# Performance work log

Hardware: AMD Instinct MI355X
Metric: run time of the kernel (lower is better)

Reference implementation:

```python
import jax, jax.numpy as jnp
import numpy as np

B = 65536
X_DIM = 362
A = 3  # action_space / number of expert dynamics MLPs


def setup_inputs() -> dict:
    key = jax.random.key(0)
    ks = jax.random.split(key, 12)
    batch_x = jax.random.normal(ks[0], (B, X_DIM), dtype=jnp.float32)
    batch_next = jax.random.normal(ks[1], (B, X_DIM), dtype=jnp.float32)
    # Plant the pointer sentinel (value 10.0) at a random in-bounds grid cell per row,
    # so that ptr-19 >= 0 and ptr+19 < X_DIM (grid width is 19).
    ptr_pos = jax.random.randint(ks[2], (B,), 20, 343)
    batch_x = batch_x.at[jnp.arange(B), ptr_pos].set(10.0)
    batch_a = jax.random.randint(ks[3], (B,), 0, A, dtype=jnp.int32)

    def lin(k, fan_in, shape):
        return (jax.random.normal(k, shape, dtype=jnp.float32) / np.sqrt(fan_in)).astype(jnp.float32)

    W1 = lin(ks[4], 6, (A, 6, 100));   b1 = jnp.zeros((A, 100), jnp.float32)
    W2 = lin(ks[5], 100, (A, 100, 400)); b2 = jnp.zeros((A, 400), jnp.float32)
    W3 = lin(ks[6], 400, (A, 400, 100)); b3 = jnp.zeros((A, 100), jnp.float32)
    W4 = lin(ks[7], 100, (A, 100, 6));  b4 = jnp.zeros((A, 6), jnp.float32)
    return {"batch_x": batch_x, "batch_next": batch_next, "batch_a": batch_a,
            "W1": W1, "b1": b1, "W2": W2, "b2": b2, "W3": W3, "b3": b3, "W4": W4, "b4": b4}


def _attend(data, ptr):
    # cell_list = [0, p, p-19 (left), p+19 (right), p-1 (above), p+1 (below)]
    zeros = jnp.zeros_like(ptr)
    idx = jnp.stack([zeros, ptr, ptr - 19, ptr + 19, ptr - 1, ptr + 1], axis=1)  # [B, 6]
    return jnp.take_along_axis(data, idx, axis=1)  # [B, 6]


def _expert(x, a, W1, b1, W2, b2, W3, b3, W4, b4):
    h = jax.nn.relu(x @ W1[a] + b1[a])
    h = jax.nn.relu(h @ W2[a] + b2[a])
    h = jax.nn.relu(h @ W3[a] + b3[a])
    return h @ W4[a] + b4[a]


def reference(batch_x, batch_next, batch_a, W1, b1, W2, b2, W3, b3, W4, b4):
    # Pointer index = first occurrence of sentinel value 10.0 per row.
    ptr = jnp.argmax(batch_x == 10.0, axis=1)  # [B]
    att = _attend(batch_x, ptr)        # [B, 6]
    att_next = _attend(batch_next, ptr)  # [B, 6]
    # Per-action routed expert MLPs (A is small and fixed): compute each expert
    # over the batch and select per-sample by action id.
    preds = jnp.zeros_like(att)
    for a in range(A):
        out_a = _expert(att, a, W1, b1, W2, b2, W3, b3, W4, b4)
        preds = jnp.where((batch_a == a)[:, None], out_a, preds)
    actual_deltas = att_next - att
    return jnp.mean((preds - actual_deltas) ** 2)
```

## Files before the change

kernel.cpp:

```cpp
#include <hip/hip_runtime.h>
#include <hip/hip_bf16.h>

#define B_ROWS 65536
#define XD 362

typedef __bf16 bf16;
typedef __attribute__((ext_vector_type(8))) __bf16 bf16x8;
typedef __attribute__((ext_vector_type(4))) float f32x4;
typedef __attribute__((ext_vector_type(2))) float f32x2;

#define MFMA16(A, Bf, C) __builtin_amdgcn_mfma_f32_16x16x32_bf16(A, Bf, C, 0, 0, 0)
#define ORDER() __builtin_amdgcn_sched_barrier(0x7F)

#define OFF_W1T   0u
#define OFF_W2T   21504u
#define OFF_W3T   340992u
#define OFF_W4T   620544u
#define OFF_CNT   632832u
#define OFF_PTR   633088u
#define OFF_ATTC  895232u
#define OFF_DELTA 4040960u
#define OFF_PART  8759552u

#define MLP_GRID 520
#define WPREP_BLOCKS 624
#define SCAN_BLOCKS 2896

__global__ __launch_bounds__(256) void k_prep(
    const float* __restrict__ W1, const float* __restrict__ b1,
    const float* __restrict__ W2, const float* __restrict__ b2,
    const float* __restrict__ W3, const float* __restrict__ b3,
    const float* __restrict__ W4, const float* __restrict__ b4,
    const float* __restrict__ x,
    bf16* __restrict__ W1t, bf16* __restrict__ W2t,
    bf16* __restrict__ W3t, bf16* __restrict__ W4t,
    int* __restrict__ cnt, int* __restrict__ ptrArr)
{
  int bx = blockIdx.x;
  if (bx >= WPREP_BLOCKS) {
    int gid = (bx - WPREP_BLOCKS) * 256 + threadIdx.x;
    const float4* x4 = (const float4*)x;
#pragma unroll
    for (int u = 0; u < 8; ++u) {
      int i = gid + u * (SCAN_BLOCKS * 256);
      float4 v = x4[i];
      if (v.x == 10.0f || v.y == 10.0f || v.z == 10.0f || v.w == 10.0f) {
        int flat = i * 4;
        if (v.x == 10.0f) ptrArr[(flat    ) / XD] = (flat    ) % XD;
        if (v.y == 10.0f) ptrArr[(flat + 1) / XD] = (flat + 1) % XD;
        if (v.z == 10.0f) ptrArr[(flat + 2) / XD] = (flat + 2) % XD;
        if (v.w == 10.0f) ptrArr[(flat + 3) / XD] = (flat + 3) % XD;
      }
    }
    return;
  }
  int i = bx * 256 + threadIdx.x;
  if (i == 0) { cnt[0] = 0; cnt[1] = 0; cnt[2] = 0; }
  if (i < 3*416*128) {
    int k = i & 127; int rn = i >> 7; int n = rn % 416; int a = rn / 416;
    float v = 0.f;
    if (n < 400) {
      if (k < 100) v = W2[(a*100 + k)*400 + n];
      else if (k == 100) v = b2[a*400 + n];
    } else if (n == 400) {
      v = (k == 100) ? 1.0f : 0.0f;
    }
    W2t[i] = (bf16)v;
  }
  if (i < 3*112*416) {
    int k = i % 416; int rn = i / 416; int n = rn % 112; int a = rn / 112;
    float v = 0.f;
    if (n < 100) {
      if (k < 400) v = W3[(a*400 + k)*100 + n];
      else if (k == 400) v = b3[a*100 + n];
    }
    W3t[i] = (bf16)v;
  }
  if (i < 3*112*32) {
    int k = i & 31; int rn = i >> 5; int n = rn % 112; int a = rn / 112;
    float v = 0.f;
    if (n < 100) {
      if (k < 6) v = W1[(a*6 + k)*100 + n];
      else if (k == 6) v = b1[a*100 + n];
    }
    W1t[i] = (bf16)v;
  }
  if (i < 3*16*128) {
    int k = i & 127; int rn = i >> 7; int n = rn & 15; int a = rn >> 4;
    float v = 0.f;
    if (n < 6) {
      if (k < 100) v = W4[(a*100 + k)*6 + n];
      else if (k == 100) v = b4[a*6 + n];
    }
    W4t[i] = (bf16)v;
  }
}

__global__ __launch_bounds__(256) void k_gather2(
    const float* __restrict__ x, const float* __restrict__ xn,
    const int* __restrict__ act, const int* __restrict__ ptrArr,
    bf16* __restrict__ attC, float* __restrict__ deltaC, int* __restrict__ cnt)
{
  int row = blockIdx.x * 256 + threadIdx.x;
  int lane = threadIdx.x & 63;
  int p = ptrArr[row];
  if (p < 20 || p > 342) p = 20;
  const float* xr = x  + (size_t)row * XD;
  const float* nr = xn + (size_t)row * XD;
  int cells[6] = {0, p, p - 19, p + 19, p - 1, p + 1};
  float av[6], dv[6];
#pragma unroll
  for (int i = 0; i < 6; ++i) {
    av[i] = xr[cells[i]];
    dv[i] = nr[cells[i]] - av[i];
  }
  int a = act[row];
  unsigned long long m0 = __ballot(a == 0);
  unsigned long long m1 = __ballot(a == 1);
  unsigned long long m2 = __ballot(a == 2);
  int b0 = 0, b1 = 0, b2 = 0;
  if (lane == 0) {
    b0 = atomicAdd(&cnt[0], (int)__popcll(m0));
    b1 = atomicAdd(&cnt[1], (int)__popcll(m1));
    b2 = atomicAdd(&cnt[2], (int)__popcll(m2));
  }
  b0 = __shfl(b0, 0); b1 = __shfl(b1, 0); b2 = __shfl(b2, 0);
  unsigned long long lt = (1ull << lane) - 1ull;
  unsigned long long ma = (a == 0) ? m0 : (a == 1) ? m1 : m2;
  int base            = (a == 0) ? b0 : (a == 1) ? b1 : b2;
  int slot = base + (int)__popcll(ma & lt);
  size_t rb = (size_t)a * B_ROWS + slot;
  bf16x8 av8;
#pragma unroll
  for (int i = 0; i < 6; ++i) av8[i] = (bf16)av[i];
  av8[6] = (bf16)1.0f;
  av8[7] = (bf16)0.0f;
  *(bf16x8*)(attC + rb * 8) = av8;
  f32x2 d01 = {dv[0], dv[1]}, d23 = {dv[2], dv[3]}, d45 = {dv[4], dv[5]};
  *(f32x2*)(deltaC + rb * 6)     = d01;
  *(f32x2*)(deltaC + rb * 6 + 2) = d23;
  *(f32x2*)(deltaC + rb * 6 + 4) = d45;
}

__global__ __launch_bounds__(256, 2) void k_mlp(
    const bf16* __restrict__ W1t, const bf16* __restrict__ W2t,
    const bf16* __restrict__ W3t, const bf16* __restrict__ W4t,
    const bf16* __restrict__ attC, const float* __restrict__ deltaC,
    const int* __restrict__ cnt, float* __restrict__ partial)
{
  int c0 = cnt[0], c1 = cnt[1], c2 = cnt[2];
  int T0 = (c0 + 127) >> 7, T1 = (c1 + 127) >> 7, T2 = (c2 + 127) >> 7;
  int b = blockIdx.x;
  int a, tile, count;
  if (b < T0)           { a = 0; tile = b;            count = c0; }
  else if (b < T0 + T1) { a = 1; tile = b - T0;       count = c1; }
  else if (b < T0 + T1 + T2) { a = 2; tile = b - T0 - T1; count = c2; }
  else { if (threadIdx.x == 0) partial[b] = 0.f; return; }
  int start = tile << 7;

  __shared__ __align__(16) bf16 h1s[4][16][136];
  __shared__ __align__(16) bf16 tr[4][2][16][56];
  __shared__ float s_part[4];
  int wv = threadIdx.x >> 6, lane = threadIdx.x & 63;
  int q = lane >> 4, c = lane & 15;

  const bf16* W1a = W1t + a * 112 * 32;
  const bf16* W2a = W2t + a * 416 * 128;
  const bf16* W3a = W3t + a * 112 * 416;
  const bf16* W4a = W4t + a * 16 * 128;

  for (int i = lane; i < 16 * 16; i += 64)
    h1s[wv][i >> 4][112 + (i & 15)] = (bf16)0.0f;

  bf16x8 A2[2][4];
#pragma unroll
  for (int mi = 0; mi < 2; ++mi) {
    bf16x8 aAtt;
#pragma unroll
    for (int i = 0; i < 8; ++i) aAtt[i] = (bf16)0.0f;
    int slot = start + wv * 32 + mi * 16 + c;
    if (q == 0 && slot < count)
      aAtt = *(const bf16x8*)(attC + ((size_t)a * B_ROWS + slot) * 8);
#pragma unroll
    for (int nt = 0; nt < 7; ++nt) {
      bf16x8 bw = *(const bf16x8*)(W1a + (nt * 16 + c) * 32 + q * 8);
      f32x4 C = {0.f, 0.f, 0.f, 0.f};
      C = MFMA16(aAtt, bw, C);
      int n = nt * 16 + c;
#pragma unroll
      for (int rg = 0; rg < 4; ++rg) {
        float v = (n < 100) ? (C[rg] > 0.f ? C[rg] : 0.f)
                            : (n == 100 ? 1.0f : 0.0f);
        h1s[wv][q * 4 + rg][n] = (bf16)v;
      }
    }
    ORDER();
#pragma unroll
    for (int tt = 0; tt < 4; ++tt)
      A2[mi][tt] = *(const bf16x8*)&h1s[wv][c][tt * 32 + q * 8];
    ORDER();
  }

  f32x4 C3[2][7];
#pragma unroll
  for (int mi = 0; mi < 2; ++mi)
#pragma unroll
    for (int i = 0; i < 7; ++i) C3[mi][i] = (f32x4){0.f, 0.f, 0.f, 0.f};

  bf16x8 b2f[2][4];
#pragma unroll
  for (int half = 0; half < 2; ++half)
#pragma unroll
    for (int tt = 0; tt < 4; ++tt)
      b2f[half][tt] = *(const bf16x8*)(W2a + (half * 16 + c) * 128 + tt * 32 + q * 8);

#pragma unroll 1
  for (int t = 0; t < 13; ++t) {
    bf16x8 w3f[7];
#pragma unroll
    for (int nt3 = 0; nt3 < 7; ++nt3)
      w3f[nt3] = *(const bf16x8*)(W3a + (nt3 * 16 + c) * 416 + t * 32 + q * 8);
    int tn = (t < 12) ? t + 1 : 12;
    bf16x8 b2n[2][4];
#pragma unroll
    for (int half = 0; half < 2; ++half)
#pragma unroll
      for (int tt = 0; tt < 4; ++tt)
        b2n[half][tt] = *(const bf16x8*)(W2a + ((2 * tn + half) * 16 + c) * 128 + tt * 32 + q * 8);
    __builtin_amdgcn_sched_barrier(0);

#pragma unroll
    for (int mi = 0; mi < 2; ++mi)
#pragma unroll
      for (int half = 0; half < 2; ++half) {
        f32x4 C = {0.f, 0.f, 0.f, 0.f};
#pragma unroll
        for (int tt = 0; tt < 4; ++tt)
          C = MFMA16(A2[mi][tt], b2f[half][tt], C);
#pragma unroll
        for (int rg = 0; rg < 4; ++rg) {
          float v = C[rg] > 0.f ? C[rg] : 0.f;
          tr[wv][mi][q * 4 + rg][half * 16 + c] = (bf16)v;
        }
      }
    ORDER();
    bf16x8 A3a = *(const bf16x8*)&tr[wv][0][c][q * 8];
    bf16x8 A3b = *(const bf16x8*)&tr[wv][1][c][q * 8];
#pragma unroll
    for (int nt3 = 0; nt3 < 7; ++nt3) {
      C3[0][nt3] = MFMA16(A3a, w3f[nt3], C3[0][nt3]);
      C3[1][nt3] = MFMA16(A3b, w3f[nt3], C3[1][nt3]);
    }
    ORDER();
#pragma unroll
    for (int half = 0; half < 2; ++half)
#pragma unroll
      for (int tt = 0; tt < 4; ++tt)
        b2f[half][tt] = b2n[half][tt];
  }

  bf16x8 b4f[4];
#pragma unroll
  for (int tt = 0; tt < 4; ++tt)
    b4f[tt] = *(const bf16x8*)(W4a + c * 128 + tt * 32 + q * 8);
  float sq = 0.f;
#pragma unroll
  for (int mi = 0; mi < 2; ++mi) {
#pragma unroll
    for (int nt3 = 0; nt3 < 7; ++nt3) {
      int n = nt3 * 16 + c;
#pragma unroll
      for (int rg = 0; rg < 4; ++rg) {
        float v = (n < 100) ? (C3[mi][nt3][rg] > 0.f ? C3[mi][nt3][rg] : 0.f)
                            : (n == 100 ? 1.0f : 0.0f);
        h1s[wv][q * 4 + rg][n] = (bf16)v;
      }
    }
    ORDER();
    f32x4 C4 = {0.f, 0.f, 0.f, 0.f};
#pragma unroll
    for (int tt = 0; tt < 4; ++tt) {
      bf16x8 A4 = *(const bf16x8*)&h1s[wv][c][tt * 32 + q * 8];
      C4 = MFMA16(A4, b4f[tt], C4);
    }
    ORDER();
    if (c < 6) {
#pragma unroll
      for (int rg = 0; rg < 4; ++rg) {
        int slot = start + wv * 32 + mi * 16 + q * 4 + rg;
        if (slot < count) {
          float d = deltaC[((size_t)a * B_ROWS + slot) * 6 + c];
          float e = C4[rg] - d;
          sq += e * e;
        }
      }
    }
  }
#pragma unroll
  for (int off = 32; off; off >>= 1) sq += __shfl_xor(sq, off);
  if (lane == 0) s_part[wv] = sq;
  __syncthreads();
  if (threadIdx.x == 0)
    partial[b] = s_part[0] + s_part[1] + s_part[2] + s_part[3];
}

__global__ __launch_bounds__(256) void k_final(
    const float* __restrict__ partial, float* __restrict__ out)
{
  __shared__ float s[4];
  int t = threadIdx.x, lane = t & 63, wv = t >> 6;
  float sum = 0.f;
  for (int i = t; i < MLP_GRID; i += 256) sum += partial[i];
#pragma unroll
  for (int off = 32; off; off >>= 1) sum += __shfl_xor(sum, off);
  if (lane == 0) s[wv] = sum;
  __syncthreads();
  if (t == 0) {
    double tot = (double)s[0] + s[1] + s[2] + s[3];
    out[0] = (float)(tot / (double)(B_ROWS * 6));
  }
}

extern "C" void kernel_launch(void* const* d_in, const int* in_sizes, int n_in,
                              void* d_out, int out_size, void* d_ws, size_t ws_size,
                              hipStream_t stream)
{
  const float* x  = (const float*)d_in[0];
  const float* xn = (const float*)d_in[1];
  const int*  act = (const int*)d_in[2];
  const float* W1 = (const float*)d_in[3];
  const float* b1 = (const float*)d_in[4];
  const float* W2 = (const float*)d_in[5];
  const float* b2 = (const float*)d_in[6];
  const float* W3 = (const float*)d_in[7];
  const float* b3 = (const float*)d_in[8];
  const float* W4 = (const float*)d_in[9];
  const float* b4 = (const float*)d_in[10];

  char* ws = (char*)d_ws;
  bf16*   W1t    = (bf16*)(ws + OFF_W1T);
  bf16*   W2t    = (bf16*)(ws + OFF_W2T);
  bf16*   W3t    = (bf16*)(ws + OFF_W3T);
  bf16*   W4t    = (bf16*)(ws + OFF_W4T);
  int*    cnt    = (int*)(ws + OFF_CNT);
  int*    ptrArr = (int*)(ws + OFF_PTR);
  bf16*   attC   = (bf16*)(ws + OFF_ATTC);
  float*  deltaC = (float*)(ws + OFF_DELTA);
  float*  part   = (float*)(ws + OFF_PART);

  k_prep<<<dim3(WPREP_BLOCKS + SCAN_BLOCKS), dim3(256), 0, stream>>>(
      W1, b1, W2, b2, W3, b3, W4, b4, x, W1t, W2t, W3t, W4t, cnt, ptrArr);
  k_gather2<<<dim3(B_ROWS / 256), dim3(256), 0, stream>>>(x, xn, act, ptrArr,
                                                          attC, deltaC, cnt);
  k_mlp<<<dim3(MLP_GRID), dim3(256), 0, stream>>>(W1t, W2t, W3t, W4t,
                                                  attC, deltaC, cnt, part);
  k_final<<<dim3(1), dim3(256), 0, stream>>>(part, (float*)d_out);
}
```

Baseline: 294.4 us.

## Halve per-wave row tile in MLP kernel and double occupancy

Each wave now processes 16 rows instead of 32, the grid doubles to 1040 blocks, and launch bounds request 4 blocks per CU instead of 2. The W2 fragment prefetch of the next iteration is dropped, so W2 is loaded inside the same iteration it is used. The aim is to cut register pressure so more waves can hide latency. The cost is that each weight fragment loaded from global/L2 is reused over half as many rows, roughly doubling weight traffic per row, and the loss of software prefetch exposes load latency.

```diff
diff --git a/kernel.cpp b/kernel.cpp
--- a/kernel.cpp
+++ b/kernel.cpp
@@ -22,7 +22,7 @@
 #define OFF_DELTA 4040960u
 #define OFF_PART  8759552u
 
-#define MLP_GRID 520
+#define MLP_GRID 1040
 #define WPREP_BLOCKS 624
 #define SCAN_BLOCKS 2896
 
@@ -142,24 +142,24 @@
   *(f32x2*)(deltaC + rb * 6 + 4) = d45;
 }
 
-__global__ __launch_bounds__(256, 2) void k_mlp(
+__global__ __launch_bounds__(256, 4) void k_mlp(
     const bf16* __restrict__ W1t, const bf16* __restrict__ W2t,
     const bf16* __restrict__ W3t, const bf16* __restrict__ W4t,
     const bf16* __restrict__ attC, const float* __restrict__ deltaC,
     const int* __restrict__ cnt, float* __restrict__ partial)
 {
   int c0 = cnt[0], c1 = cnt[1], c2 = cnt[2];
-  int T0 = (c0 + 127) >> 7, T1 = (c1 + 127) >> 7, T2 = (c2 + 127) >> 7;
+  int T0 = (c0 + 63) >> 6, T1 = (c1 + 63) >> 6, T2 = (c2 + 63) >> 6;
   int b = blockIdx.x;
   int a, tile, count;
   if (b < T0)           { a = 0; tile = b;            count = c0; }
   else if (b < T0 + T1) { a = 1; tile = b - T0;       count = c1; }
   else if (b < T0 + T1 + T2) { a = 2; tile = b - T0 - T1; count = c2; }
   else { if (threadIdx.x == 0) partial[b] = 0.f; return; }
-  int start = tile << 7;
+  int start = tile << 6;
 
   __shared__ __align__(16) bf16 h1s[4][16][136];
-  __shared__ __align__(16) bf16 tr[4][2][16][56];
+  __shared__ __align__(16) bf16 tr[4][16][40];
   __shared__ float s_part[4];
   int wv = threadIdx.x >> 6, lane = threadIdx.x & 63;
   int q = lane >> 4, c = lane & 15;
@@ -172,47 +172,35 @@
   for (int i = lane; i < 16 * 16; i += 64)
     h1s[wv][i >> 4][112 + (i & 15)] = (bf16)0.0f;
 
-  bf16x8 A2[2][4];
-#pragma unroll
-  for (int mi = 0; mi < 2; ++mi) {
-    bf16x8 aAtt;
-#pragma unroll
-    for (int i = 0; i < 8; ++i) aAtt[i] = (bf16)0.0f;
-    int slot = start + wv * 32 + mi * 16 + c;
-    if (q == 0 && slot < count)
-      aAtt = *(const bf16x8*)(attC + ((size_t)a * B_ROWS + slot) * 8);
-#pragma unroll
-    for (int nt = 0; nt < 7; ++nt) {
-      bf16x8 bw = *(const bf16x8*)(W1a + (nt * 16 + c) * 32 + q * 8);
-      f32x4 C = {0.f, 0.f, 0.f, 0.f};
-      C = MFMA16(aAtt, bw, C);
-      int n = nt * 16 + c;
-#pragma unroll
-      for (int rg = 0; rg < 4; ++rg) {
-        float v = (n < 100) ? (C[rg] > 0.f ? C[rg] : 0.f)
-                            : (n == 100 ? 1.0f : 0.0f);
-        h1s[wv][q * 4 + rg][n] = (bf16)v;
-      }
-    }
-    ORDER();
-#pragma unroll
-    for (int tt = 0; tt < 4; ++tt)
-      A2[mi][tt] = *(const bf16x8*)&h1s[wv][c][tt * 32 + q * 8];
-    ORDER();
-  }
-
-  f32x4 C3[2][7];
-#pragma unroll
-  for (int mi = 0; mi < 2; ++mi)
-#pragma unroll
-    for (int i = 0; i < 7; ++i) C3[mi][i] = (f32x4){0.f, 0.f, 0.f, 0.f};
-
-  bf16x8 b2f[2][4];
-#pragma unroll
-  for (int half = 0; half < 2; ++half)
-#pragma unroll
-    for (int tt = 0; tt < 4; ++tt)
-      b2f[half][tt] = *(const bf16x8*)(W2a + (half * 16 + c) * 128 + tt * 32 + q * 8);
+  bf16x8 aAtt;
+#pragma unroll
+  for (int i = 0; i < 8; ++i) aAtt[i] = (bf16)0.0f;
+  int slot = start + wv * 16 + c;
+  if (q == 0 && slot < count)
+    aAtt = *(const bf16x8*)(attC + ((size_t)a * B_ROWS + slot) * 8);
+#pragma unroll
+  for (int nt = 0; nt < 7; ++nt) {
+    bf16x8 bw = *(const bf16x8*)(W1a + (nt * 16 + c) * 32 + q * 8);
+    f32x4 C = {0.f, 0.f, 0.f, 0.f};
+    C = MFMA16(aAtt, bw, C);
+    int n = nt * 16 + c;
+#pragma unroll
+    for (int rg = 0; rg < 4; ++rg) {
+      float v = (n < 100) ? (C[rg] > 0.f ? C[rg] : 0.f)
+                          : (n == 100 ? 1.0f : 0.0f);
+      h1s[wv][q * 4 + rg][n] = (bf16)v;
+    }
+  }
+  ORDER();
+  bf16x8 A2[4];
+#pragma unroll
+  for (int tt = 0; tt < 4; ++tt)
+    A2[tt] = *(const bf16x8*)&h1s[wv][c][tt * 32 + q * 8];
+  ORDER();
+
+  f32x4 C3[7];
+#pragma unroll
+  for (int i = 0; i < 7; ++i) C3[i] = (f32x4){0.f, 0.f, 0.f, 0.f};
 
 #pragma unroll 1
   for (int t = 0; t < 13; ++t) {
@@ -220,43 +208,32 @@
 #pragma unroll
     for (int nt3 = 0; nt3 < 7; ++nt3)
       w3f[nt3] = *(const bf16x8*)(W3a + (nt3 * 16 + c) * 416 + t * 32 + q * 8);
-    int tn = (t < 12) ? t + 1 : 12;
-    bf16x8 b2n[2][4];
+    bf16x8 b2f[2][4];
 #pragma unroll
     for (int half = 0; half < 2; ++half)
 #pragma unroll
       for (int tt = 0; tt < 4; ++tt)
-        b2n[half][tt] = *(const bf16x8*)(W2a + ((2 * tn + half) * 16 + c) * 128 + tt * 32 + q * 8);
+        b2f[half][tt] = *(const bf16x8*)(W2a + ((2 * t + half) * 16 + c) * 128 + tt * 32 + q * 8);
     __builtin_amdgcn_sched_barrier(0);
 
 #pragma unroll
-    for (int mi = 0; mi < 2; ++mi)
-#pragma unroll
-      for (int half = 0; half < 2; ++half) {
-        f32x4 C = {0.f, 0.f, 0.f, 0.f};
-#pragma unroll
-        for (int tt = 0; tt < 4; ++tt)
-          C = MFMA16(A2[mi][tt], b2f[half][tt], C);
-#pragma unroll
-        for (int rg = 0; rg < 4; ++rg) {
-          float v = C[rg] > 0.f ? C[rg] : 0.f;
-          tr[wv][mi][q * 4 + rg][half * 16 + c] = (bf16)v;
-        }
+    for (int half = 0; half < 2; ++half) {
+      f32x4 C = {0.f, 0.f, 0.f, 0.f};
+#pragma unroll
+      for (int tt = 0; tt < 4; ++tt)
+        C = MFMA16(A2[tt], b2f[half][tt], C);
+#pragma unroll
+      for (int rg = 0; rg < 4; ++rg) {
+        float v = C[rg] > 0.f ? C[rg] : 0.f;
+        tr[wv][q * 4 + rg][half * 16 + c] = (bf16)v;
       }
+    }
     ORDER();
-    bf16x8 A3a = *(const bf16x8*)&tr[wv][0][c][q * 8];
-    bf16x8 A3b = *(const bf16x8*)&tr[wv][1][c][q * 8];
-#pragma unroll
-    for (int nt3 = 0; nt3 < 7; ++nt3) {
-      C3[0][nt3] = MFMA16(A3a, w3f[nt3], C3[0][nt3]);
-      C3[1][nt3] = MFMA16(A3b, w3f[nt3], C3[1][nt3]);
-    }
+    bf16x8 A3 = *(const bf16x8*)&tr[wv][c][q * 8];
+#pragma unroll
+    for (int nt3 = 0; nt3 < 7; ++nt3)
+      C3[nt3] = MFMA16(A3, w3f[nt3], C3[nt3]);
     ORDER();
-#pragma unroll
-    for (int half = 0; half < 2; ++half)
-#pragma unroll
-      for (int tt = 0; tt < 4; ++tt)
-        b2f[half][tt] = b2n[half][tt];
   }
 
   bf16x8 b4f[4];
@@ -265,34 +242,31 @@
     b4f[tt] = *(const bf16x8*)(W4a + c * 128 + tt * 32 + q * 8);
   float sq = 0.f;
 #pragma unroll
-  for (int mi = 0; mi < 2; ++mi) {
-#pragma unroll
-    for (int nt3 = 0; nt3 < 7; ++nt3) {
-      int n = nt3 * 16 + c;
-#pragma unroll
-      for (int rg = 0; rg < 4; ++rg) {
-        float v = (n < 100) ? (C3[mi][nt3][rg] > 0.f ? C3[mi][nt3][rg] : 0.f)
-                            : (n == 100 ? 1.0f : 0.0f);
-        h1s[wv][q * 4 + rg][n] = (bf16)v;
-      }
-    }
-    ORDER();
-    f32x4 C4 = {0.f, 0.f, 0.f, 0.f};
-#pragma unroll
-    for (int tt = 0; tt < 4; ++tt) {
-      bf16x8 A4 = *(const bf16x8*)&h1s[wv][c][tt * 32 + q * 8];
-      C4 = MFMA16(A4, b4f[tt], C4);
-    }
-    ORDER();
-    if (c < 6) {
-#pragma unroll
-      for (int rg = 0; rg < 4; ++rg) {
-        int slot = start + wv * 32 + mi * 16 + q * 4 + rg;
-        if (slot < count) {
-          float d = deltaC[((size_t)a * B_ROWS + slot) * 6 + c];
-          float e = C4[rg] - d;
-          sq += e * e;
-        }
+  for (int nt3 = 0; nt3 < 7; ++nt3) {
+    int n = nt3 * 16 + c;
+#pragma unroll
+    for (int rg = 0; rg < 4; ++rg) {
+      float v = (n < 100) ? (C3[nt3][rg] > 0.f ? C3[nt3][rg] : 0.f)
+                          : (n == 100 ? 1.0f : 0.0f);
+      h1s[wv][q * 4 + rg][n] = (bf16)v;
+    }
+  }
+  ORDER();
+  f32x4 C4 = {0.f, 0.f, 0.f, 0.f};
+#pragma unroll
+  for (int tt = 0; tt < 4; ++tt) {
+    bf16x8 A4 = *(const bf16x8*)&h1s[wv][c][tt * 32 + q * 8];
+    C4 = MFMA16(A4, b4f[tt], C4);
+  }
+  ORDER();
+  if (c < 6) {
+#pragma unroll
+    for (int rg = 0; rg < 4; ++rg) {
+      int slot2 = start + wv * 16 + q * 4 + rg;
+      if (slot2 < count) {
+        float d = deltaC[((size_t)a * B_ROWS + slot2) * 6 + c];
+        float e = C4[rg] - d;
+        sq += e * e;
       }
     }
   }
```

New measurement: 324.9 us. 1.1x slower.

## Stage W2/W3 chunks into double-buffered LDS via async global_load_lds with swizzle

Applied to the files above, without the earlier changes.

Each block now cooperatively copies the per-step W2 and W3 weight chunks into a double-buffered shared-memory area using direct global-to-LDS loads, instead of every wave fetching them from global memory into registers. The prep kernel rewrites the W2/W3 layouts with XOR-swizzled k-groups and a chunk-major W3 layout so the LDS reads avoid bank conflicts. This removes the fourfold redundant global/L2 weight traffic across waves, but it adds a block-wide barrier every iteration and uses more LDS, which could reduce occupancy.

```diff
diff --git a/kernel.cpp b/kernel.cpp
--- a/kernel.cpp
+++ b/kernel.cpp
@@ -26,6 +26,7 @@
 #define WPREP_BLOCKS 624
 #define SCAN_BLOCKS 2896
 
+
 __global__ __launch_bounds__(256) void k_prep(
     const float* __restrict__ W1, const float* __restrict__ b1,
     const float* __restrict__ W2, const float* __restrict__ b2,
@@ -57,7 +58,9 @@
   int i = bx * 256 + threadIdx.x;
   if (i == 0) { cnt[0] = 0; cnt[1] = 0; cnt[2] = 0; }
   if (i < 3*416*128) {
-    int k = i & 127; int rn = i >> 7; int n = rn % 416; int a = rn / 416;
+    int e = i & 7; int g = (i >> 3) & 15;
+    int rn = i >> 7; int n = rn % 416; int a = rn / 416;
+    int k = ((g ^ (n & 7)) << 3) | e;
     float v = 0.f;
     if (n < 400) {
       if (k < 100) v = W2[(a*100 + k)*400 + n];
@@ -67,8 +70,10 @@
     }
     W2t[i] = (bf16)v;
   }
-  if (i < 3*112*416) {
-    int k = i % 416; int rn = i / 416; int n = rn % 112; int a = rn / 112;
+  if (i < 3*13*112*32) {
+    int e = i & 7; int g = (i >> 3) & 3;
+    int n = (i >> 5) % 112; int tc = ((i >> 5) / 112) % 13; int a = i / (13*112*32);
+    int k = tc * 32 + ((g ^ (n & 3)) << 3) + e;
     float v = 0.f;
     if (n < 100) {
       if (k < 400) v = W3[(a*400 + k)*100 + n];
@@ -158,16 +163,37 @@
   else { if (threadIdx.x == 0) partial[b] = 0.f; return; }
   int start = tile << 7;
 
+  __shared__ __align__(16) bf16 bufW2[2][32][128];
+  __shared__ __align__(16) bf16 bufW3[2][112][32];
   __shared__ __align__(16) bf16 h1s[4][16][136];
   __shared__ __align__(16) bf16 tr[4][2][16][56];
   __shared__ float s_part[4];
   int wv = threadIdx.x >> 6, lane = threadIdx.x & 63;
   int q = lane >> 4, c = lane & 15;
+  int cx7 = c & 7, cx3 = c & 3;
 
   const bf16* W1a = W1t + a * 112 * 32;
   const bf16* W2a = W2t + a * 416 * 128;
-  const bf16* W3a = W3t + a * 112 * 416;
+  const bf16* W3a = W3t + a * 13 * 112 * 32;
   const bf16* W4a = W4t + a * 16 * 128;
+
+  auto stage = [&](int tn) {
+    const char* s2 = (const char*)W2a + tn * 8192;
+    const char* s3 = (const char*)W3a + tn * 7168;
+    char* d2 = (char*)&bufW2[tn & 1][0][0];
+    char* d3 = (char*)&bufW3[tn & 1][0][0];
+#pragma unroll
+    for (int id = wv; id < 15; id += 4) {
+      const char* src = (id < 8) ? s2 + id * 1024 + lane * 16
+                                 : s3 + (id - 8) * 1024 + lane * 16;
+      char* dst = (id < 8) ? d2 + id * 1024 : d3 + (id - 8) * 1024;
+      __builtin_amdgcn_global_load_lds(
+          (const __attribute__((address_space(1))) unsigned int*)src,
+          (__attribute__((address_space(3))) unsigned int*)dst, 16, 0, 0);
+    }
+  };
+
+  stage(0);
 
   for (int i = lane; i < 16 * 16; i += 64)
     h1s[wv][i >> 4][112 + (i & 15)] = (bf16)0.0f;
@@ -207,27 +233,26 @@
 #pragma unroll
     for (int i = 0; i < 7; ++i) C3[mi][i] = (f32x4){0.f, 0.f, 0.f, 0.f};
 
-  bf16x8 b2f[2][4];
-#pragma unroll
-  for (int half = 0; half < 2; ++half)
-#pragma unroll
-    for (int tt = 0; tt < 4; ++tt)
-      b2f[half][tt] = *(const bf16x8*)(W2a + (half * 16 + c) * 128 + tt * 32 + q * 8);
+  __syncthreads();
 
 #pragma unroll 1
   for (int t = 0; t < 13; ++t) {
+    if (t < 12) stage(t + 1);
+    __builtin_amdgcn_sched_barrier(0);
+
+    const bf16* cw2 = &bufW2[t & 1][0][0];
+    const bf16* cw3 = &bufW3[t & 1][0][0];
     bf16x8 w3f[7];
 #pragma unroll
     for (int nt3 = 0; nt3 < 7; ++nt3)
-      w3f[nt3] = *(const bf16x8*)(W3a + (nt3 * 16 + c) * 416 + t * 32 + q * 8);
-    int tn = (t < 12) ? t + 1 : 12;
-    bf16x8 b2n[2][4];
+      w3f[nt3] = *(const bf16x8*)(cw3 + (nt3 * 16 + c) * 32 + ((q ^ cx3) << 3));
+    bf16x8 b2f[2][4];
 #pragma unroll
     for (int half = 0; half < 2; ++half)
 #pragma unroll
       for (int tt = 0; tt < 4; ++tt)
-        b2n[half][tt] = *(const bf16x8*)(W2a + ((2 * tn + half) * 16 + c) * 128 + tt * 32 + q * 8);
-    __builtin_amdgcn_sched_barrier(0);
+        b2f[half][tt] = *(const bf16x8*)(cw2 + (half * 16 + c) * 128 +
+                                         ((((tt << 2) + q) ^ cx7) << 3));
 
 #pragma unroll
     for (int mi = 0; mi < 2; ++mi)
@@ -252,11 +277,7 @@
       C3[1][nt3] = MFMA16(A3b, w3f[nt3], C3[1][nt3]);
     }
     ORDER();
-#pragma unroll
-    for (int half = 0; half < 2; ++half)
-#pragma unroll
-      for (int tt = 0; tt < 4; ++tt)
-        b2f[half][tt] = b2n[half][tt];
+    __syncthreads();
   }
 
   bf16x8 b4f[4];
```

Result: faster. 272.9 us (-7.3%).
